# Performance work log

Measured on AMD Instinct MI355X. Metric: run time of the kernel, lower is better.

The kernel has to match this reference:

```python
import jax, jax.numpy as jnp
import numpy as np

PHI = 1.618033988749895  # golden ratio
TWO_PI = 2.0 * np.pi
LUT_SIZE = 4096
ALPHA = 1.0


def _wrap(t):
    # wrap_time_periodic: wrap phase into [0, 2*pi)
    return jnp.mod(t, TWO_PI)


def _make_lut():
    ang = (TWO_PI / LUT_SIZE) * jnp.arange(LUT_SIZE, dtype=jnp.float32)
    return jnp.sin(ang), jnp.cos(ang)


def _lut_sin_cos(theta, sin_t, cos_t):
    # 4096-entry LUT sin/cos: quantize wrapped phase to table index
    idx = jnp.floor(_wrap(theta) * (LUT_SIZE / TWO_PI)).astype(jnp.int32) % LUT_SIZE
    return sin_t[idx], cos_t[idx]


def setup_inputs() -> dict:
    key = jax.random.key(0)
    ks = jax.random.split(key, 9)
    B, S, D, N, L, V, SIG = 128, 1024, 256, 1024, 2, 32000, 256
    return {
        "input_ids": jax.random.randint(ks[0], (B, S), 0, V),
        "token_emb": jax.random.normal(ks[1], (V, 2 * D), dtype=jnp.float32) * 0.01,
        "win_r": jax.random.normal(ks[2], (L, D, N), dtype=jnp.float32) / np.sqrt(D),
        "win_i": jax.random.normal(ks[3], (L, D, N), dtype=jnp.float32) / np.sqrt(D),
        "wout_r": jax.random.normal(ks[4], (L, N, D), dtype=jnp.float32) / np.sqrt(N),
        "wout_i": jax.random.normal(ks[5], (L, N, D), dtype=jnp.float32) / np.sqrt(N),
        "omega": jax.random.normal(ks[6], (L, N), dtype=jnp.float32),
        "outp_r": jax.random.normal(ks[7], (D, SIG), dtype=jnp.float32) / np.sqrt(D),
        "outp_i": jax.random.normal(ks[8], (D, SIG), dtype=jnp.float32) / np.sqrt(D),
    }


def reference(input_ids, token_emb, win_r, win_i, wout_r, wout_i, omega, outp_r, outp_i):
    sin_t, cos_t = _make_lut()
    B, S = input_ids.shape
    D = token_emb.shape[1] // 2
    L, N = omega.shape

    emb = token_emb[input_ids]                      # [B, S, 2D]
    w_seq = jnp.transpose(emb[..., :D], (1, 0, 2))  # [S, B, D] time-major
    b_seq = jnp.transpose(emb[..., D:], (1, 0, 2))  # [S, B, D]
    t_seq = jnp.arange(S, dtype=jnp.float32)

    h0 = jnp.zeros((B, D), jnp.float32)
    s0 = jnp.zeros((L, B, N), jnp.float32)

    def step(carry, xs):
        h_r, h_i, s_r, s_i, _, _ = carry
        w, b, t = xs
        # euler_transform: LUT-based complex rotation, no residuals
        wavelength = 1.0 + jnp.abs(w)
        t_phi = _wrap(t * PHI)
        th_r = h_r / wavelength + b + t_phi
        th_i = h_i / wavelength + b + t_phi
        sr, cr = _lut_sin_cos(th_r, sin_t, cos_t)
        si, ci = _lut_sin_cos(th_i, sin_t, cos_t)
        h_r_new = cr * ci - sr * si
        h_i_new = cr * si + sr * ci
        x_r, x_i = h_r_new, h_i_new
        srs, sis = [], []
        for l in range(L):  # small fixed layer loop
            # complex projection into echo chamber
            u_r = x_r @ win_r[l] - x_i @ win_i[l]
            u_i = x_r @ win_i[l] + x_i @ win_r[l]
            # rotate reservoir state by per-neuron frequency + PHI time phase
            sn, cn = _lut_sin_cos(omega[l] + t * PHI, sin_t, cos_t)
            nr = ALPHA * (s_r[l] * cn - s_i[l] * sn) + u_r
            ni = ALPHA * (s_r[l] * sn + s_i[l] * cn) + u_i
            # complex projection back to d_model
            x_r = nr @ wout_r[l] - ni @ wout_i[l]
            x_i = nr @ wout_i[l] + ni @ wout_r[l]
            srs.append(nr)
            sis.append(ni)
        return (h_r_new, h_i_new, jnp.stack(srs), jnp.stack(sis), x_r, x_i), None

    carry0 = (h0, h0, s0, s0, h0, h0)
    (_, _, _, _, x_r, x_i), _ = jax.lax.scan(step, carry0, (w_seq, b_seq, t_seq))

    # output_proj: ComplexLinear(d_model, num_signals, bias=False); logits_real + logits_imag
    lr = x_r @ outp_r - x_i @ outp_i
    li = x_r @ outp_i + x_i @ outp_r
    return lr + li
```

## Files before the change

### kernel.cpp

```cpp
#include <hip/hip_runtime.h>

#define S_LEN 1024
#define BB 128
#define DD 256
#define NN 1024
#define TWO_K 512
#define TWO_N 2048

typedef _Float16 half8 __attribute__((ext_vector_type(8)));
typedef _Float16 half4 __attribute__((ext_vector_type(4)));
typedef float f32x4 __attribute__((ext_vector_type(4)));

__device__ __forceinline__ float wrap2pi(float x) {
  float r = fmodf(x, 6.283185307179586f);
  if (r < 0.f) r += 6.283185307179586f;
  return r;
}
__device__ __forceinline__ int lut_index(float th) {
  float w = wrap2pi(th);
  return ((int)floorf(w * 651.8986469044033f)) & 4095;
}
__device__ __forceinline__ float q12(float th) {
  const float y = floorf(th * 651.8986469044033f) * 0.000244140625f;
  return y - floorf(y);
}

__global__ __launch_bounds__(256) void k_h(const int* __restrict__ ids,
                                           const float* __restrict__ emb,
                                           float* __restrict__ hstate,
                                           _Float16* __restrict__ X0,
                                           int t0, int CH) {
  __shared__ __align__(16) float ebuf[2][8][2][256];
  __shared__ float tphi_s[1024];
  const int tid = threadIdx.x;
  const int lane = tid & 63;
  const int wv = tid >> 6;
  for (int i = tid; i < CH; i += 256)
    tphi_s[i] = wrap2pi((float)(t0 + i) * 1.618033988749895f);

  const int b = blockIdx.x;
  const int d = tid;
  const int* __restrict__ idrow = ids + b * S_LEN + t0;
  const int NST = CH >> 3;

#pragma unroll
  for (int q = 0; q < 2; ++q) {
    const int j = wv * 2 + q;
    const int id = idrow[j];
    const float* src = emb + (size_t)id * 512 + lane * 4;
    __builtin_amdgcn_global_load_lds((const __attribute__((address_space(1))) void*)src,
                                     (__attribute__((address_space(3))) void*)(&ebuf[0][j][0][0]), 16, 0, 0);
    __builtin_amdgcn_global_load_lds((const __attribute__((address_space(1))) void*)(src + 256),
                                     (__attribute__((address_space(3))) void*)(&ebuf[0][j][1][0]), 16, 0, 0);
  }

  float hr, hi;
  if (t0 == 0) { hr = 0.f; hi = 0.f; }
  else { float2 h = ((const float2*)hstate)[b * DD + d]; hr = h.x; hi = h.y; }

  int buf = 0;
  __syncthreads();

  for (int st = 0; st < NST; ++st) {
    if (st + 1 < NST) {
#pragma unroll
      for (int q = 0; q < 2; ++q) {
        const int j = wv * 2 + q;
        const int id = idrow[(st + 1) * 8 + j];
        const float* src = emb + (size_t)id * 512 + lane * 4;
        __builtin_amdgcn_global_load_lds((const __attribute__((address_space(1))) void*)src,
                                         (__attribute__((address_space(3))) void*)(&ebuf[buf ^ 1][j][0][0]), 16, 0, 0);
        __builtin_amdgcn_global_load_lds((const __attribute__((address_space(1))) void*)(src + 256),
                                         (__attribute__((address_space(3))) void*)(&ebuf[buf ^ 1][j][1][0]), 16, 0, 0);
      }
    }
    float rwl[8], bvt[8];
#pragma unroll
    for (int j = 0; j < 8; ++j) {
      const float w  = ebuf[buf][j][0][d];
      const float bv = ebuf[buf][j][1][d];
      rwl[j] = 1.0f / (1.f + fabsf(w));
      bvt[j] = bv + tphi_s[st * 8 + j];
    }
#pragma unroll
    for (int j = 0; j < 8; ++j) {
      const int tt = st * 8 + j;
      const float thr = fmaf(hr, rwl[j], bvt[j]);
      const float thi = fmaf(hi, rwl[j], bvt[j]);
      const float fr = q12(thr);
      const float fi = q12(thi);
      const float sr = __builtin_amdgcn_sinf(fr), cr = __builtin_amdgcn_cosf(fr);
      const float si = __builtin_amdgcn_sinf(fi), ci = __builtin_amdgcn_cosf(fi);
      hr = cr * ci - sr * si;
      hi = cr * si + sr * ci;
      union { unsigned int u; _Float16 h2[2]; } pk;
      pk.h2[0] = (_Float16)hr; pk.h2[1] = (_Float16)hi;
      *(((unsigned int*)(X0 + (size_t)(tt * BB + b) * TWO_K)) + d) = pk.u;
    }
    __syncthreads();
    buf ^= 1;
  }
  ((float2*)hstate)[b * DD + d] = make_float2(hr, hi);
}

__global__ __launch_bounds__(256) void k_rot(const float* __restrict__ omega,
                                             float2* __restrict__ C0, float2* __restrict__ D0,
                                             float2* __restrict__ D1, float2* __restrict__ C1last) {
  const int blk = blockIdx.x;
  const int l = blk >> 10, n = blk & (NN - 1);
  const int tid = threadIdx.x;
  const int lane = tid & 63;
  const int wid = tid >> 6;
  const float om = omega[l * NN + n];

  int pre[4];
  int own = 0;
  const int tb = tid * 4;
#pragma unroll
  for (int j = 0; j < 4; ++j) {
    own += lut_index(om + (float)(tb + j) * 1.618033988749895f);
    pre[j] = own;
  }
  int v = own;
#pragma unroll
  for (int off = 1; off < 64; off <<= 1) {
    int u = __shfl_up(v, off);
    if (lane >= off) v += u;
  }
  __shared__ int wsum[4];
  if (lane == 63) wsum[wid] = v;
  __syncthreads();
  int woff = 0;
#pragma unroll
  for (int w = 0; w < 4; ++w) woff += (w < wid) ? wsum[w] : 0;
  const int excl = woff + v - own;

#pragma unroll
  for (int j = 0; j < 4; ++j) {
    const int t = tb + j;
    const int idx = (excl + pre[j]) & 4095;
    const float s = sinf(0.0015339807878856412f * (float)idx);
    const float c = cosf(0.0015339807878856412f * (float)idx);
    if (l == 0) {
      C0[t * NN + n] = make_float2(c, s);
      D0[t * NN + n] = make_float2(c, -s);
    } else {
      D1[t * NN + n] = make_float2(c, -s);
      if (t == S_LEN - 1) C1last[n] = make_float2(c, s);
    }
  }
}

__global__ __launch_bounds__(256, 2) void k_gemm(const _Float16* __restrict__ A,
                                                 const _Float16* __restrict__ BT,
                                                 _Float16* __restrict__ C,
                                                 int M, int N, int K, int nxlog2,
                                                 const float2* __restrict__ rot) {
  __shared__ __align__(16) _Float16 As[128 * 64];
  __shared__ __align__(16) _Float16 Bs[128 * 64];
  const int tid = threadIdx.x;
  const int lane = tid & 63;
  const int wave = tid >> 6;
  const int wm = wave >> 1;
  const int wn = wave & 1;

  const int cpx = gridDim.x >> 3;
  const int bid = blockIdx.x;
  const int swz = (bid & 7) * cpx + (bid >> 3);
  const int bx = swz & ((1 << nxlog2) - 1);
  const int by = swz >> nxlog2;
  const int m0 = by * 128;
  const int n0 = bx * 128;

  const int srow = lane >> 3;
  const int schunk = (lane & 7) ^ srow;

  f32x4 acc[4][4] = {};

  for (int kt = 0; kt < K; kt += 64) {
#pragma unroll
    for (int j = 0; j < 4; ++j) {
      const int c = wave * 4 + j;
      const int row = c * 8 + srow;
      const _Float16* srcA = A + (size_t)(m0 + row) * K + kt + schunk * 8;
      __builtin_amdgcn_global_load_lds((const __attribute__((address_space(1))) void*)srcA,
                                       (__attribute__((address_space(3))) void*)(As + c * 512), 16, 0, 0);
      const _Float16* srcB = BT + (size_t)(n0 + row) * K + kt + schunk * 8;
      __builtin_amdgcn_global_load_lds((const __attribute__((address_space(1))) void*)srcB,
                                       (__attribute__((address_space(3))) void*)(Bs + c * 512), 16, 0, 0);
    }
    __syncthreads();
#pragma unroll
    for (int ks = 0; ks < 2; ++ks) {
      half8 af[4], bf[4];
#pragma unroll
      for (int mr = 0; mr < 4; ++mr) {
        const int ar = wm * 64 + mr * 16 + (lane & 15);
        const int p = ((ks * 4) + (lane >> 4)) ^ (ar & 7);
        af[mr] = *(const half8*)(As + ar * 64 + p * 8);
      }
#pragma unroll
      for (int nr = 0; nr < 4; ++nr) {
        const int br = wn * 64 + nr * 16 + (lane & 15);
        const int p = ((ks * 4) + (lane >> 4)) ^ (br & 7);
        bf[nr] = *(const half8*)(Bs + br * 64 + p * 8);
      }
#pragma unroll
      for (int mr = 0; mr < 4; ++mr)
#pragma unroll
        for (int nr = 0; nr < 4; ++nr)
          acc[mr][nr] = __builtin_amdgcn_mfma_f32_16x16x32_f16(af[mr], bf[nr], acc[mr][nr], 0, 0, 0);
    }
    __syncthreads();
  }

  const int halfN = N >> 1;
  const int t = by;
#pragma unroll
  for (int mr = 0; mr < 4; ++mr)
#pragma unroll
    for (int nr = 0; nr < 4; ++nr) {
      const int col = n0 + wn * 64 + nr * 16 + (lane & 15);
      const int rbase = m0 + wm * 64 + mr * 16 + ((lane >> 4) << 2);
      float2 dr = make_float2(1.f, 0.f);
      if (rot) dr = rot[(size_t)t * halfN + (col >> 1)];
#pragma unroll
      for (int j = 0; j < 4; ++j) {
        float v = acc[mr][nr][j];
        if (rot) {
          const float pv = __shfl_xor(v, 1);
          v = (lane & 1) ? (dr.x * v + dr.y * pv) : (dr.x * v - dr.y * pv);
        }
        C[(size_t)(rbase + j) * N + col] = (_Float16)v;
      }
    }
}

#define SUF 8
__global__ __launch_bounds__(256) void k_scan(_Float16* __restrict__ V,
                                              const float2* __restrict__ C0c,
                                              float2* __restrict__ ZS, int CH, int first) {
  const int gid = blockIdx.x * 256 + threadIdx.x;
  const int npair = gid & (NN / 2 - 1);
  const int b = gid >> 9;
  const int n = npair * 2;
  float zr0, zi0, zr1, zi1;
  if (first) { zr0 = zi0 = zr1 = zi1 = 0.f; }
  else {
    float4 z = *(const float4*)(ZS + (size_t)b * NN + n);
    zr0 = z.x; zi0 = z.y; zr1 = z.z; zi1 = z.w;
  }
  uint2 vb[SUF], vn[SUF];
  float4 cb[SUF], cn[SUF];
#pragma unroll
  for (int j = 0; j < SUF; ++j) {
    vb[j] = *(const uint2*)(((const unsigned int*)(V + (size_t)(j * BB + b) * TWO_N)) + n);
    cb[j] = *(const float4*)(C0c + (size_t)j * NN + n);
  }
  for (int st = 0; st < CH; st += SUF) {
    const bool more = (st + SUF) < CH;
    if (more) {
#pragma unroll
      for (int j = 0; j < SUF; ++j) {
        vn[j] = *(const uint2*)(((const unsigned int*)(V + (size_t)((st + SUF + j) * BB + b) * TWO_N)) + n);
        cn[j] = *(const float4*)(C0c + (size_t)(st + SUF + j) * NN + n);
      }
    }
#pragma unroll
    for (int j = 0; j < SUF; ++j) {
      union { unsigned int u; _Float16 h2[2]; } a, c;
      a.u = vb[j].x; c.u = vb[j].y;
      zr0 += (float)a.h2[0]; zi0 += (float)a.h2[1];
      zr1 += (float)c.h2[0]; zi1 += (float)c.h2[1];
      const float4 cc = cb[j];
      a.h2[0] = (_Float16)(cc.x * zr0 - cc.y * zi0);
      a.h2[1] = (_Float16)(cc.x * zi0 + cc.y * zr0);
      c.h2[0] = (_Float16)(cc.z * zr1 - cc.w * zi1);
      c.h2[1] = (_Float16)(cc.z * zi1 + cc.w * zr1);
      *(uint2*)(((unsigned int*)(V + (size_t)((st + j) * BB + b) * TWO_N)) + n) = make_uint2(a.u, c.u);
    }
#pragma unroll
    for (int j = 0; j < SUF; ++j) { vb[j] = vn[j]; cb[j] = cn[j]; }
  }
  *(float4*)(ZS + (size_t)b * NN + n) = make_float4(zr0, zi0, zr1, zi1);
}

__global__ __launch_bounds__(256) void k_reduce(const _Float16* __restrict__ U,
                                                float* __restrict__ s1, int CH, int first) {
  const int gid = blockIdx.x * 256 + threadIdx.x;
  const int g = gid & (TWO_N / 4 - 1);
  const int b = gid >> 9;
  const int np = g * 4;
  f32x4 acc;
  if (first) {
#pragma unroll
    for (int j = 0; j < 4; ++j) acc[j] = 0.f;
  } else {
    acc = *(const f32x4*)(s1 + (size_t)b * TWO_N + np);
  }
  half4 vb[SUF], vn[SUF];
#pragma unroll
  for (int j = 0; j < SUF; ++j)
    vb[j] = *(const half4*)(U + (size_t)(j * BB + b) * TWO_N + np);
  for (int st = 0; st < CH; st += SUF) {
    const bool more = (st + SUF) < CH;
    if (more) {
#pragma unroll
      for (int j = 0; j < SUF; ++j)
        vn[j] = *(const half4*)(U + (size_t)((st + SUF + j) * BB + b) * TWO_N + np);
    }
#pragma unroll
    for (int j = 0; j < SUF; ++j) {
#pragma unroll
      for (int q = 0; q < 4; ++q) acc[q] += (float)vb[j][q];
    }
#pragma unroll
    for (int j = 0; j < SUF; ++j) vb[j] = vn[j];
  }
  *(f32x4*)(s1 + (size_t)b * TWO_N + np) = acc;
}

__global__ __launch_bounds__(256) void k_s1c(const float* __restrict__ s1,
                                             const float2* __restrict__ C1last,
                                             float* __restrict__ s1c) {
  const int gid = blockIdx.x * 256 + threadIdx.x;
  const int n = gid & (NN - 1);
  const int b = gid >> 10;
  const float sr = s1[b * TWO_N + 2 * n], si = s1[b * TWO_N + 2 * n + 1];
  const float2 c = C1last[n];
  s1c[b * TWO_N + 2 * n]     = c.x * sr - c.y * si;
  s1c[b * TWO_N + 2 * n + 1] = c.x * si + c.y * sr;
}

__global__ __launch_bounds__(256) void k_tail(const float* __restrict__ A,
                                              const float* __restrict__ BT,
                                              float* __restrict__ C, int M, int N, int K) {
  const int wave = threadIdx.x >> 6;
  const int lane = threadIdx.x & 63;
  const int o = blockIdx.x * 4 + wave;
  if (o >= M * N) return;
  const int row = o / N;
  const int col = o - row * N;
  const float4* __restrict__ a4 = (const float4*)(A + (size_t)row * K);
  const float4* __restrict__ b4 = (const float4*)(BT + (size_t)col * K);
  float acc = 0.f;
  const int nit = K >> 8;
  for (int it = 0; it < nit; ++it) {
    const float4 av = a4[it * 64 + lane];
    const float4 bv = b4[it * 64 + lane];
    acc = fmaf(av.x, bv.x, acc);
    acc = fmaf(av.y, bv.y, acc);
    acc = fmaf(av.z, bv.z, acc);
    acc = fmaf(av.w, bv.w, acc);
  }
#pragma unroll
  for (int s = 32; s >= 1; s >>= 1) acc += __shfl_xor(acc, s);
  if (lane == 0) C[o] = acc;
}

__global__ __launch_bounds__(256) void k_prep_in(const float* __restrict__ r, const float* __restrict__ im,
                                                 _Float16* __restrict__ dst) {
  const int gid = blockIdx.x * 256 + threadIdx.x;
  const int n = gid & (NN - 1);
  const int k = gid >> 10;
  const float rv = r[(size_t)k * NN + n], iv = im[(size_t)k * NN + n];
  const size_t base = (size_t)(2 * n) * TWO_K + 2 * k;
  dst[base] = (_Float16)rv;              dst[base + 1] = (_Float16)(-iv);
  dst[base + TWO_K] = (_Float16)iv;      dst[base + TWO_K + 1] = (_Float16)rv;
}
__global__ __launch_bounds__(256) void k_prep_out(const float* __restrict__ r, const float* __restrict__ im,
                                                  _Float16* __restrict__ dst) {
  const int gid = blockIdx.x * 256 + threadIdx.x;
  const int d = gid & (DD - 1);
  const int n = gid >> 8;
  const float rv = r[(size_t)n * DD + d], iv = im[(size_t)n * DD + d];
  const size_t base = (size_t)(2 * d) * TWO_N + 2 * n;
  dst[base] = (_Float16)rv;              dst[base + 1] = (_Float16)(-iv);
  dst[base + TWO_N] = (_Float16)iv;      dst[base + TWO_N + 1] = (_Float16)rv;
}
__global__ __launch_bounds__(256) void k_prep_wout1T(const float* __restrict__ r, const float* __restrict__ im,
                                                     float* __restrict__ dstT) {
  const int gid = blockIdx.x * 256 + threadIdx.x;
  const int n = gid & (NN - 1);
  const int d = gid >> 10;
  const float rv = r[(size_t)n * DD + d], iv = im[(size_t)n * DD + d];
  const size_t b0 = (size_t)(2 * d) * TWO_N + 2 * n;
  const size_t b1 = (size_t)(2 * d + 1) * TWO_N + 2 * n;
  dstT[b0] = rv;     dstT[b0 + 1] = -iv;
  dstT[b1] = iv;     dstT[b1 + 1] = rv;
}
__global__ __launch_bounds__(256) void k_prep_finT(const float* __restrict__ pr, const float* __restrict__ pi_,
                                                   float* __restrict__ dstT) {
  const int gid = blockIdx.x * 256 + threadIdx.x;
  const int d = gid & (DD - 1);
  const int s = gid >> 8;
  const float a = pr[(size_t)d * 256 + s], b = pi_[(size_t)d * 256 + s];
  dstT[(size_t)s * TWO_K + 2 * d] = a + b;
  dstT[(size_t)s * TWO_K + 2 * d + 1] = a - b;
}

extern "C" void kernel_launch(void* const* d_in, const int* in_sizes, int n_in,
                              void* d_out, int out_size, void* d_ws, size_t ws_size,
                              hipStream_t stream) {
  const int* ids      = (const int*)d_in[0];
  const float* emb    = (const float*)d_in[1];
  const float* win_r  = (const float*)d_in[2];
  const float* win_i  = (const float*)d_in[3];
  const float* wout_r = (const float*)d_in[4];
  const float* wout_i = (const float*)d_in[5];
  const float* omega  = (const float*)d_in[6];
  const float* outp_r = (const float*)d_in[7];
  const float* outp_i = (const float*)d_in[8];

  char* ws = (char*)d_ws;
  size_t off = 0;
  auto alloc = [&](size_t bytes) { void* p = ws + off; off += (bytes + 255) & ~(size_t)255; return p; };

  float2* C0     = (float2*)alloc((size_t)S_LEN * NN * 8);
  float2* D0     = (float2*)alloc((size_t)S_LEN * NN * 8);
  float2* D1     = (float2*)alloc((size_t)S_LEN * NN * 8);
  float2* C1last = (float2*)alloc((size_t)NN * 8);
  float2* ZS     = (float2*)alloc((size_t)BB * NN * 8);
  float* hstate  = (float*)alloc((size_t)BB * DD * 2 * 4);
  float* s1      = (float*)alloc((size_t)BB * TWO_N * 4);
  float* s1c     = (float*)alloc((size_t)BB * TWO_N * 4);
  float* xt      = (float*)alloc((size_t)BB * TWO_K * 4);
  _Float16* BTin0  = (_Float16*)alloc((size_t)TWO_N * TWO_K * 2);
  _Float16* BTout0 = (_Float16*)alloc((size_t)TWO_K * TWO_N * 2);
  _Float16* BTin1  = (_Float16*)alloc((size_t)TWO_N * TWO_K * 2);
  float* Wout1T = (float*)alloc((size_t)TWO_K * TWO_N * 4);
  float* WfinT  = (float*)alloc((size_t)256 * TWO_K * 4);
  const size_t fixed = off;

  int CH = 1024;
  while (CH > 32) {
    size_t need = fixed + (size_t)CH * BB * 2 * (TWO_K + TWO_N) + 2 * 256;
    if (need <= ws_size) break;
    CH >>= 1;
  }
  _Float16* X0 = (_Float16*)alloc((size_t)CH * BB * TWO_K * 2);
  _Float16* VB = (_Float16*)alloc((size_t)CH * BB * TWO_N * 2);
  _Float16* Yc = X0;

  k_rot<<<2 * NN, 256, 0, stream>>>(omega, C0, D0, D1, C1last);
  k_prep_in<<<DD * NN / 256, 256, 0, stream>>>(win_r, win_i, BTin0);
  k_prep_in<<<DD * NN / 256, 256, 0, stream>>>(win_r + (size_t)DD * NN, win_i + (size_t)DD * NN, BTin1);
  k_prep_out<<<NN * DD / 256, 256, 0, stream>>>(wout_r, wout_i, BTout0);
  k_prep_wout1T<<<NN * DD / 256, 256, 0, stream>>>(wout_r + (size_t)NN * DD, wout_i + (size_t)NN * DD, Wout1T);
  k_prep_finT<<<DD * 256 / 256, 256, 0, stream>>>(outp_r, outp_i, WfinT);

  const int nchunks = S_LEN / CH;
  for (int c = 0; c < nchunks; ++c) {
    const int t0 = c * CH;
    const int M = CH * BB;
    k_h<<<BB, 256, 0, stream>>>(ids, emb, hstate, X0, t0, CH);
    const int nb1 = (TWO_N / 128) * (M / 128);
    k_gemm<<<nb1, 256, 0, stream>>>(X0, BTin0, VB, M, TWO_N, TWO_K, 4, D0 + (size_t)t0 * NN);
    k_scan<<<BB * (NN / 2) / 256, 256, 0, stream>>>(VB, C0 + (size_t)t0 * NN, ZS, CH, c == 0);
    const int nb2 = (TWO_K / 128) * (M / 128);
    k_gemm<<<nb2, 256, 0, stream>>>(VB, BTout0, Yc, M, TWO_K, TWO_N, 2, nullptr);
    k_gemm<<<nb1, 256, 0, stream>>>(Yc, BTin1, VB, M, TWO_N, TWO_K, 4, D1 + (size_t)t0 * NN);
    k_reduce<<<BB * (TWO_N / 4) / 256, 256, 0, stream>>>(VB, s1, CH, c == 0);
  }

  k_s1c<<<BB * NN / 256, 256, 0, stream>>>(s1, C1last, s1c);
  k_tail<<<BB * TWO_K / 4, 256, 0, stream>>>(s1c, Wout1T, xt, BB, TWO_K, TWO_N);
  k_tail<<<BB * 256 / 4, 256, 0, stream>>>(xt, WfinT, (float*)d_out, BB, 256, TWO_K);
}
```

Baseline: 1.636 ms.

## Rewrite GEMM with 256x256 tiles, 512 threads and 4-stage async LDS pipeline

Reworks the fp16 MFMA GEMM to use 256x256 block tiles with 8 waves, a 32-wide K step, and a four-buffer LDS ring. Global-to-LDS loads are issued three stages ahead and gated with explicit vmcnt waits instead of full syncthreads. MFMA issue is wrapped in s_setprio. The aim is to overlap memory latency with compute and raise arithmetic intensity per block, at the cost of fewer blocks per launch and one wave-group per CU. The rotation epilogue row index is remapped so each 128-row half picks its own time step.

```diff
diff --git a/kernel.cpp b/kernel.cpp
--- a/kernel.cpp
+++ b/kernel.cpp
@@ -151,77 +151,99 @@
   }
 }
 
-__global__ __launch_bounds__(256, 2) void k_gemm(const _Float16* __restrict__ A,
+#define GBK 32
+#define ABUFH (256 * GBK)
+#define BUFH  (2 * ABUFH)
+__global__ __launch_bounds__(512, 1) void k_gemm(const _Float16* __restrict__ A,
                                                  const _Float16* __restrict__ BT,
                                                  _Float16* __restrict__ C,
                                                  int M, int N, int K, int nxlog2,
                                                  const float2* __restrict__ rot) {
-  __shared__ __align__(16) _Float16 As[128 * 64];
-  __shared__ __align__(16) _Float16 Bs[128 * 64];
+  __shared__ __align__(16) _Float16 lds[4 * BUFH];
   const int tid = threadIdx.x;
   const int lane = tid & 63;
-  const int wave = tid >> 6;
-  const int wm = wave >> 1;
-  const int wn = wave & 1;
-
+  const int w = tid >> 6;
+  const int wm = w >> 2;
+  const int wn = w & 3;
   const int cpx = gridDim.x >> 3;
   const int bid = blockIdx.x;
   const int swz = (bid & 7) * cpx + (bid >> 3);
   const int bx = swz & ((1 << nxlog2) - 1);
   const int by = swz >> nxlog2;
-  const int m0 = by * 128;
-  const int n0 = bx * 128;
-
-  const int srow = lane >> 3;
-  const int schunk = (lane & 7) ^ srow;
-
-  f32x4 acc[4][4] = {};
-
-  for (int kt = 0; kt < K; kt += 64) {
-#pragma unroll
-    for (int j = 0; j < 4; ++j) {
-      const int c = wave * 4 + j;
-      const int row = c * 8 + srow;
-      const _Float16* srcA = A + (size_t)(m0 + row) * K + kt + schunk * 8;
-      __builtin_amdgcn_global_load_lds((const __attribute__((address_space(1))) void*)srcA,
-                                       (__attribute__((address_space(3))) void*)(As + c * 512), 16, 0, 0);
-      const _Float16* srcB = BT + (size_t)(n0 + row) * K + kt + schunk * 8;
-      __builtin_amdgcn_global_load_lds((const __attribute__((address_space(1))) void*)srcB,
-                                       (__attribute__((address_space(3))) void*)(Bs + c * 512), 16, 0, 0);
-    }
-    __syncthreads();
-#pragma unroll
-    for (int ks = 0; ks < 2; ++ks) {
-      half8 af[4], bf[4];
-#pragma unroll
-      for (int mr = 0; mr < 4; ++mr) {
-        const int ar = wm * 64 + mr * 16 + (lane & 15);
-        const int p = ((ks * 4) + (lane >> 4)) ^ (ar & 7);
-        af[mr] = *(const half8*)(As + ar * 64 + p * 8);
-      }
-#pragma unroll
-      for (int nr = 0; nr < 4; ++nr) {
-        const int br = wn * 64 + nr * 16 + (lane & 15);
-        const int p = ((ks * 4) + (lane >> 4)) ^ (br & 7);
-        bf[nr] = *(const half8*)(Bs + br * 64 + p * 8);
-      }
-#pragma unroll
-      for (int mr = 0; mr < 4; ++mr)
-#pragma unroll
-        for (int nr = 0; nr < 4; ++nr)
-          acc[mr][nr] = __builtin_amdgcn_mfma_f32_16x16x32_f16(af[mr], bf[nr], acc[mr][nr], 0, 0, 0);
-    }
-    __syncthreads();
+  const int m0 = by * 256;
+  const int n0 = bx * 256;
+  const int nt = K >> 5;
+
+  const int srow4 = lane >> 2;
+  const int sq = lane & 3;
+
+  auto STAGE = [&](int p) {
+    _Float16* buf = lds + (size_t)(p & 3) * BUFH;
+    const int kt = p << 5;
+#pragma unroll
+    for (int j = 0; j < 2; ++j) {
+      const int row = j * 128 + w * 16 + srow4;
+      const int q = sq ^ ((row >> 1) & 3);
+      const _Float16* src = A + (size_t)(m0 + row) * K + kt + q * 8;
+      __builtin_amdgcn_global_load_lds((const __attribute__((address_space(1))) void*)src,
+                                       (__attribute__((address_space(3))) void*)(buf + (j * 128 + w * 16) * GBK),
+                                       16, 0, 0);
+    }
+#pragma unroll
+    for (int j = 0; j < 2; ++j) {
+      const int row = j * 128 + w * 16 + srow4;
+      const int q = sq ^ ((row >> 1) & 3);
+      const _Float16* src = BT + (size_t)(n0 + row) * K + kt + q * 8;
+      __builtin_amdgcn_global_load_lds((const __attribute__((address_space(1))) void*)src,
+                                       (__attribute__((address_space(3))) void*)(buf + ABUFH + (j * 128 + w * 16) * GBK),
+                                       16, 0, 0);
+    }
+  };
+
+  STAGE(0); STAGE(1); STAGE(2);
+
+  f32x4 acc[8][4] = {};
+
+  for (int i = 0; i < nt; ++i) {
+    if (i + 2 < nt)      asm volatile("s_waitcnt vmcnt(8)" ::: "memory");
+    else if (i + 1 < nt) asm volatile("s_waitcnt vmcnt(4)" ::: "memory");
+    else                 asm volatile("s_waitcnt vmcnt(0)" ::: "memory");
+    __builtin_amdgcn_s_barrier();
+    asm volatile("" ::: "memory");
+    if (i + 3 < nt) STAGE(i + 3);
+
+    const _Float16* As = lds + (size_t)(i & 3) * BUFH;
+    const _Float16* Bs = As + ABUFH;
+    const int p0 = lane >> 4;
+    half8 bf[4];
+#pragma unroll
+    for (int nr = 0; nr < 4; ++nr) {
+      const int br = wn * 64 + nr * 16 + (lane & 15);
+      bf[nr] = *(const half8*)(Bs + br * GBK + (p0 ^ ((br >> 1) & 3)) * 8);
+    }
+    half8 af[8];
+#pragma unroll
+    for (int mr = 0; mr < 8; ++mr) {
+      const int ar = wm * 128 + mr * 16 + (lane & 15);
+      af[mr] = *(const half8*)(As + ar * GBK + (p0 ^ ((ar >> 1) & 3)) * 8);
+    }
+    __builtin_amdgcn_s_setprio(1);
+#pragma unroll
+    for (int mr = 0; mr < 8; ++mr)
+#pragma unroll
+      for (int nr = 0; nr < 4; ++nr)
+        acc[mr][nr] = __builtin_amdgcn_mfma_f32_16x16x32_f16(af[mr], bf[nr], acc[mr][nr], 0, 0, 0);
+    __builtin_amdgcn_s_setprio(0);
   }
 
   const int halfN = N >> 1;
-  const int t = by;
-#pragma unroll
-  for (int mr = 0; mr < 4; ++mr)
+  const int t = by * 2 + wm;
+#pragma unroll
+  for (int mr = 0; mr < 8; ++mr)
 #pragma unroll
     for (int nr = 0; nr < 4; ++nr) {
       const int col = n0 + wn * 64 + nr * 16 + (lane & 15);
-      const int rbase = m0 + wm * 64 + mr * 16 + ((lane >> 4) << 2);
+      const int rbase = m0 + wm * 128 + mr * 16 + ((lane >> 4) << 2);
       float2 dr = make_float2(1.f, 0.f);
       if (rot) dr = rot[(size_t)t * halfN + (col >> 1)];
 #pragma unroll
@@ -454,12 +476,12 @@
     const int t0 = c * CH;
     const int M = CH * BB;
     k_h<<<BB, 256, 0, stream>>>(ids, emb, hstate, X0, t0, CH);
-    const int nb1 = (TWO_N / 128) * (M / 128);
-    k_gemm<<<nb1, 256, 0, stream>>>(X0, BTin0, VB, M, TWO_N, TWO_K, 4, D0 + (size_t)t0 * NN);
+    const int nb1 = (M / 256) * (TWO_N / 256);
+    k_gemm<<<nb1, 512, 0, stream>>>(X0, BTin0, VB, M, TWO_N, TWO_K, 3, D0 + (size_t)t0 * NN);
     k_scan<<<BB * (NN / 2) / 256, 256, 0, stream>>>(VB, C0 + (size_t)t0 * NN, ZS, CH, c == 0);
-    const int nb2 = (TWO_K / 128) * (M / 128);
-    k_gemm<<<nb2, 256, 0, stream>>>(VB, BTout0, Yc, M, TWO_K, TWO_N, 2, nullptr);
-    k_gemm<<<nb1, 256, 0, stream>>>(Yc, BTin1, VB, M, TWO_N, TWO_K, 4, D1 + (size_t)t0 * NN);
+    const int nb2 = (M / 256) * (TWO_K / 256);
+    k_gemm<<<nb2, 512, 0, stream>>>(VB, BTout0, Yc, M, TWO_K, TWO_N, 1, nullptr);
+    k_gemm<<<nb1, 512, 0, stream>>>(Yc, BTin1, VB, M, TWO_N, TWO_K, 3, D1 + (size_t)t0 * NN);
     k_reduce<<<BB * (TWO_N / 4) / 256, 256, 0, stream>>>(VB, s1, CH, c == 0);
   }
 
```

Result: slower. 1.764 ms (+7.8%).

## Double-buffer LDS tiles in GEMM to overlap global loads with MFMA

Applied to the files above, without the earlier changes.

The GEMM kernel now uses two LDS buffers and issues the global-to-LDS loads for tile i+2 while tile i is being computed. It waits with explicit vmcnt counts and raw s_barrier calls instead of a full __syncthreads. The aim is to hide global memory latency behind MFMA work. LDS use doubles to 64KB per block, which may lower occupancy under launch_bounds(256,2). The manual waitcnt logic is also fragile. The grid-size expressions are only reordered.

```diff
diff --git a/kernel.cpp b/kernel.cpp
--- a/kernel.cpp
+++ b/kernel.cpp
@@ -156,8 +156,7 @@
                                                  _Float16* __restrict__ C,
                                                  int M, int N, int K, int nxlog2,
                                                  const float2* __restrict__ rot) {
-  __shared__ __align__(16) _Float16 As[128 * 64];
-  __shared__ __align__(16) _Float16 Bs[128 * 64];
+  __shared__ __align__(16) _Float16 lds[2][2][128 * 64];
   const int tid = threadIdx.x;
   const int lane = tid & 63;
   const int wave = tid >> 6;
@@ -171,25 +170,40 @@
   const int by = swz >> nxlog2;
   const int m0 = by * 128;
   const int n0 = bx * 128;
+  const int nt = K >> 6;
 
   const int srow = lane >> 3;
   const int schunk = (lane & 7) ^ srow;
 
-  f32x4 acc[4][4] = {};
-
-  for (int kt = 0; kt < K; kt += 64) {
+  auto STAGE = [&](int p) {
+    _Float16* Asb = &lds[p & 1][0][0];
+    _Float16* Bsb = &lds[p & 1][1][0];
+    const int kt = p << 6;
 #pragma unroll
     for (int j = 0; j < 4; ++j) {
       const int c = wave * 4 + j;
       const int row = c * 8 + srow;
       const _Float16* srcA = A + (size_t)(m0 + row) * K + kt + schunk * 8;
       __builtin_amdgcn_global_load_lds((const __attribute__((address_space(1))) void*)srcA,
-                                       (__attribute__((address_space(3))) void*)(As + c * 512), 16, 0, 0);
+                                       (__attribute__((address_space(3))) void*)(Asb + c * 512), 16, 0, 0);
       const _Float16* srcB = BT + (size_t)(n0 + row) * K + kt + schunk * 8;
       __builtin_amdgcn_global_load_lds((const __attribute__((address_space(1))) void*)srcB,
-                                       (__attribute__((address_space(3))) void*)(Bs + c * 512), 16, 0, 0);
-    }
-    __syncthreads();
+                                       (__attribute__((address_space(3))) void*)(Bsb + c * 512), 16, 0, 0);
+    }
+  };
+
+  STAGE(0);
+  STAGE(1);
+
+  f32x4 acc[4][4] = {};
+
+  for (int i = 0; i < nt; ++i) {
+    if (i + 1 < nt) asm volatile("s_waitcnt vmcnt(8)" ::: "memory");
+    else            asm volatile("s_waitcnt vmcnt(0)" ::: "memory");
+    __builtin_amdgcn_s_barrier();
+    asm volatile("" ::: "memory");
+    const _Float16* As = &lds[i & 1][0][0];
+    const _Float16* Bs = &lds[i & 1][1][0];
 #pragma unroll
     for (int ks = 0; ks < 2; ++ks) {
       half8 af[4], bf[4];
@@ -211,7 +225,10 @@
         for (int nr = 0; nr < 4; ++nr)
           acc[mr][nr] = __builtin_amdgcn_mfma_f32_16x16x32_f16(af[mr], bf[nr], acc[mr][nr], 0, 0, 0);
     }
-    __syncthreads();
+    asm volatile("" ::: "memory");
+    __builtin_amdgcn_s_barrier();
+    asm volatile("" ::: "memory");
+    if (i + 2 < nt) STAGE(i + 2);
   }
 
   const int halfN = N >> 1;
@@ -454,10 +471,10 @@
     const int t0 = c * CH;
     const int M = CH * BB;
     k_h<<<BB, 256, 0, stream>>>(ids, emb, hstate, X0, t0, CH);
-    const int nb1 = (TWO_N / 128) * (M / 128);
+    const int nb1 = (M / 128) * (TWO_N / 128);
     k_gemm<<<nb1, 256, 0, stream>>>(X0, BTin0, VB, M, TWO_N, TWO_K, 4, D0 + (size_t)t0 * NN);
     k_scan<<<BB * (NN / 2) / 256, 256, 0, stream>>>(VB, C0 + (size_t)t0 * NN, ZS, CH, c == 0);
-    const int nb2 = (TWO_K / 128) * (M / 128);
+    const int nb2 = (M / 128) * (TWO_K / 128);
     k_gemm<<<nb2, 256, 0, stream>>>(VB, BTout0, Yc, M, TWO_K, TWO_N, 2, nullptr);
     k_gemm<<<nb1, 256, 0, stream>>>(Yc, BTin1, VB, M, TWO_N, TWO_K, 4, D1 + (size_t)t0 * NN);
     k_reduce<<<BB * (TWO_N / 4) / 256, 256, 0, stream>>>(VB, s1, CH, c == 0);
```

Result: slower. 1.873 ms (+14.5%).

## Fuse timestep reduction into layer-1 GEMM epilogue via float atomics

Applied to the files above, without the earlier changes.

Removes the separate k_reduce kernel and instead accumulates each layer-1 GEMM output directly into the per-batch state sum s1 with atomicAdd, after zeroing s1 once up front. This avoids writing the full layer-1 activation buffer to memory and reading it back for the time reduction. In exchange every output element becomes a global float atomic with heavy contention across timesteps, and summation order becomes nondeterministic.

```diff
diff --git a/kernel.cpp b/kernel.cpp
--- a/kernel.cpp
+++ b/kernel.cpp
@@ -155,7 +155,8 @@
                                                  const _Float16* __restrict__ BT,
                                                  _Float16* __restrict__ C,
                                                  int M, int N, int K, int nxlog2,
-                                                 const float2* __restrict__ rot) {
+                                                 const float2* __restrict__ rot,
+                                                 float* __restrict__ s1red) {
   __shared__ __align__(16) _Float16 As[128 * 64];
   __shared__ __align__(16) _Float16 Bs[128 * 64];
   const int tid = threadIdx.x;
@@ -231,7 +232,11 @@
           const float pv = __shfl_xor(v, 1);
           v = (lane & 1) ? (dr.x * v + dr.y * pv) : (dr.x * v - dr.y * pv);
         }
-        C[(size_t)(rbase + j) * N + col] = (_Float16)v;
+        if (s1red) {
+          atomicAdd(&s1red[(size_t)((rbase + j) & (BB - 1)) * N + col], v);
+        } else {
+          C[(size_t)(rbase + j) * N + col] = (_Float16)v;
+        }
       }
     }
 }
@@ -285,39 +290,9 @@
   *(float4*)(ZS + (size_t)b * NN + n) = make_float4(zr0, zi0, zr1, zi1);
 }
 
-__global__ __launch_bounds__(256) void k_reduce(const _Float16* __restrict__ U,
-                                                float* __restrict__ s1, int CH, int first) {
-  const int gid = blockIdx.x * 256 + threadIdx.x;
-  const int g = gid & (TWO_N / 4 - 1);
-  const int b = gid >> 9;
-  const int np = g * 4;
-  f32x4 acc;
-  if (first) {
-#pragma unroll
-    for (int j = 0; j < 4; ++j) acc[j] = 0.f;
-  } else {
-    acc = *(const f32x4*)(s1 + (size_t)b * TWO_N + np);
-  }
-  half4 vb[SUF], vn[SUF];
-#pragma unroll
-  for (int j = 0; j < SUF; ++j)
-    vb[j] = *(const half4*)(U + (size_t)(j * BB + b) * TWO_N + np);
-  for (int st = 0; st < CH; st += SUF) {
-    const bool more = (st + SUF) < CH;
-    if (more) {
-#pragma unroll
-      for (int j = 0; j < SUF; ++j)
-        vn[j] = *(const half4*)(U + (size_t)((st + SUF + j) * BB + b) * TWO_N + np);
-    }
-#pragma unroll
-    for (int j = 0; j < SUF; ++j) {
-#pragma unroll
-      for (int q = 0; q < 4; ++q) acc[q] += (float)vb[j][q];
-    }
-#pragma unroll
-    for (int j = 0; j < SUF; ++j) vb[j] = vn[j];
-  }
-  *(f32x4*)(s1 + (size_t)b * TWO_N + np) = acc;
+__global__ __launch_bounds__(256) void k_zero(float* __restrict__ p) {
+  const int gid = blockIdx.x * 256 + threadIdx.x;
+  ((float4*)p)[gid] = make_float4(0.f, 0.f, 0.f, 0.f);
 }
 
 __global__ __launch_bounds__(256) void k_s1c(const float* __restrict__ s1,
@@ -448,19 +423,22 @@
   k_prep_out<<<NN * DD / 256, 256, 0, stream>>>(wout_r, wout_i, BTout0);
   k_prep_wout1T<<<NN * DD / 256, 256, 0, stream>>>(wout_r + (size_t)NN * DD, wout_i + (size_t)NN * DD, Wout1T);
   k_prep_finT<<<DD * 256 / 256, 256, 0, stream>>>(outp_r, outp_i, WfinT);
+  k_zero<<<BB * TWO_N / 4 / 256, 256, 0, stream>>>(s1);
 
   const int nchunks = S_LEN / CH;
   for (int c = 0; c < nchunks; ++c) {
     const int t0 = c * CH;
     const int M = CH * BB;
     k_h<<<BB, 256, 0, stream>>>(ids, emb, hstate, X0, t0, CH);
-    const int nb1 = (TWO_N / 128) * (M / 128);
-    k_gemm<<<nb1, 256, 0, stream>>>(X0, BTin0, VB, M, TWO_N, TWO_K, 4, D0 + (size_t)t0 * NN);
+    const int nb1 = (M / 128) * (TWO_N / 128);
+    k_gemm<<<nb1, 256, 0, stream>>>(X0, BTin0, VB, M, TWO_N, TWO_K, 4,
+                                    D0 + (size_t)t0 * NN, nullptr);
     k_scan<<<BB * (NN / 2) / 256, 256, 0, stream>>>(VB, C0 + (size_t)t0 * NN, ZS, CH, c == 0);
-    const int nb2 = (TWO_K / 128) * (M / 128);
-    k_gemm<<<nb2, 256, 0, stream>>>(VB, BTout0, Yc, M, TWO_K, TWO_N, 2, nullptr);
-    k_gemm<<<nb1, 256, 0, stream>>>(Yc, BTin1, VB, M, TWO_N, TWO_K, 4, D1 + (size_t)t0 * NN);
-    k_reduce<<<BB * (TWO_N / 4) / 256, 256, 0, stream>>>(VB, s1, CH, c == 0);
+    const int nb2 = (M / 128) * (TWO_K / 128);
+    k_gemm<<<nb2, 256, 0, stream>>>(VB, BTout0, Yc, M, TWO_K, TWO_N, 2,
+                                    nullptr, nullptr);
+    k_gemm<<<nb1, 256, 0, stream>>>(Yc, BTin1, VB, M, TWO_N, TWO_K, 4,
+                                    D1 + (size_t)t0 * NN, s1);
   }
 
   k_s1c<<<BB * NN / 256, 256, 0, stream>>>(s1, C1last, s1c);
```

New measurement: 2.209 ms. +35.0%, slower.
